# Kernel tuning notes

Hardware: AMD Instinct MI355X
Metric: run time of the kernel (lower is better)

The kernel has to match this reference:

```python
import jax, jax.numpy as jnp
import numpy as np
import math

VOCAB = 32000
D_MODEL = 1024
CTX = 2048
B, T = 4, 2048
NUM_Q_HEADS = 16
NUM_KV_GROUPS = 4
HEAD_DIM = D_MODEL // NUM_Q_HEADS          # 64
REP = NUM_Q_HEADS // NUM_KV_GROUPS         # queries per KV group = 4
HALF = D_MODEL // 2                        # token/pos embedding width


def setup_inputs() -> dict:
    key = jax.random.key(0)
    ks = jax.random.split(key, 12)
    s = 0.02
    idx = jax.random.randint(ks[0], (B, T), 0, VOCAB, dtype=jnp.int32)
    mask = jnp.tril(jnp.ones((T, T), dtype=jnp.int32))  # causal mask, 0 = blocked
    return {
        "idx": idx,
        "mask": mask,
        "tok_table": jax.random.normal(ks[1], (VOCAB, HALF), jnp.float32) * s,
        "pos_table": jax.random.normal(ks[2], (CTX, HALF), jnp.float32) * s,
        "W_q": jax.random.normal(ks[3], (D_MODEL, D_MODEL), jnp.float32) * s,
        "b_q": jnp.zeros((D_MODEL,), jnp.float32),
        "W_k": jax.random.normal(ks[4], (D_MODEL, NUM_KV_GROUPS * HEAD_DIM), jnp.float32) * s,
        "b_k": jnp.zeros((NUM_KV_GROUPS * HEAD_DIM,), jnp.float32),
        "W_v": jax.random.normal(ks[5], (D_MODEL, NUM_KV_GROUPS * HEAD_DIM), jnp.float32) * s,
        "b_v": jnp.zeros((NUM_KV_GROUPS * HEAD_DIM,), jnp.float32),
        "W_o": jax.random.normal(ks[6], (D_MODEL, D_MODEL), jnp.float32) * s,
        "b_o": jnp.zeros((D_MODEL,), jnp.float32),
    }


def reference(idx, mask, tok_table, pos_table, W_q, b_q, W_k, b_k, W_v, b_v, W_o, b_o):
    Bd, Td = idx.shape
    # token + position embedding, concatenated along feature dim -> [B, T, D_MODEL]
    tok_emb = tok_table[idx]                              # [B, T, HALF]
    pos_emb = pos_table[jnp.arange(Td)]                   # [T, HALF]
    x = jnp.concatenate([tok_emb, jnp.broadcast_to(pos_emb, (Bd, Td, HALF))], axis=-1)

    # GQA projections
    Q = (x @ W_q + b_q).reshape(Bd, Td, NUM_Q_HEADS, HEAD_DIM).transpose(0, 2, 1, 3)   # [B,H,T,D]
    K = (x @ W_k + b_k).reshape(Bd, Td, NUM_KV_GROUPS, HEAD_DIM).transpose(0, 2, 1, 3) # [B,G,T,D]
    V = (x @ W_v + b_v).reshape(Bd, Td, NUM_KV_GROUPS, HEAD_DIM).transpose(0, 2, 1, 3)
    # repeat_interleave KV groups to match query heads (naive GQA expansion)
    K = jnp.repeat(K, REP, axis=1)                        # [B,H,T,D]
    V = jnp.repeat(V, REP, axis=1)

    scale = 1.0 / math.sqrt(HEAD_DIM)
    scores = jnp.einsum('bhqd,bhkd->bhqk', Q, K) * scale  # [B,H,T,T]
    scores = jnp.where(mask == 0, jnp.float32(-1e9), scores)
    probs = jax.nn.softmax(scores, axis=-1)
    attn = jnp.einsum('bhqk,bhkd->bhqd', probs, V)        # [B,H,T,D]
    attn = attn.transpose(0, 2, 1, 3).reshape(Bd, Td, D_MODEL)
    return attn @ W_o + b_o
```

## Files before the change

kernel.cpp:

```cpp
#include <hip/hip_runtime.h>

typedef unsigned short u16;
typedef __attribute__((ext_vector_type(8))) short bf16x8;
typedef __attribute__((ext_vector_type(4))) float f32x4;

__device__ __forceinline__ u16 f2bf(float f) {
  union { float f; unsigned u; } x; x.f = f;
  unsigned r = x.u + 0x7fffu + ((x.u >> 16) & 1u);
  return (u16)(r >> 16);
}
__device__ __forceinline__ float bf2f(u16 u) {
  union { unsigned u; float f; } x; x.u = ((unsigned)u) << 16;
  return x.f;
}

#define GLOAD_LDS16(gp, lp)                                              \
  __builtin_amdgcn_global_load_lds(                                      \
      (const __attribute__((address_space(1))) unsigned int*)(gp),       \
      (__attribute__((address_space(3))) unsigned int*)(lp), 16, 0, 0)

__global__ __launch_bounds__(256) void transpose_w(const float* __restrict__ in,
                                                   u16* __restrict__ out, int N) {
  __shared__ float tile[32][33];
  const int n0 = blockIdx.x * 32, k0 = blockIdx.y * 32;
  const int tx = threadIdx.x & 31, ty = threadIdx.x >> 5;
#pragma unroll
  for (int i = 0; i < 4; ++i) {
    int k = k0 + ty + i * 8;
    tile[ty + i * 8][tx] = in[(size_t)k * N + n0 + tx];
  }
  __syncthreads();
#pragma unroll
  for (int i = 0; i < 4; ++i) {
    int n = n0 + ty + i * 8;
    out[(size_t)n * 1024 + k0 + tx] = f2bf(tile[tx][ty + i * 8]);
  }
}

__global__ __launch_bounds__(256) void embed_kernel(const int* __restrict__ idx,
                                                    const float* __restrict__ tok,
                                                    const float* __restrict__ pos,
                                                    u16* __restrict__ x) {
  const int r = blockIdx.x;
  const int t = r & 2047;
  const int tok_id = idx[r];
  const int c = threadIdx.x * 4;
  float4 v;
  if (c < 512)
    v = *(const float4*)&tok[(size_t)tok_id * 512 + c];
  else
    v = *(const float4*)&pos[(size_t)t * 512 + (c - 512)];
  ushort4 o;
  o.x = f2bf(v.x); o.y = f2bf(v.y); o.z = f2bf(v.z); o.w = f2bf(v.w);
  *(ushort4*)&x[(size_t)r * 1024 + c] = o;
}

__global__ __launch_bounds__(256) void gemm_qkv(const u16* __restrict__ A,
                                                const u16* __restrict__ Bt,
                                                const float* __restrict__ bq,
                                                const float* __restrict__ bk,
                                                const float* __restrict__ bv,
                                                u16* __restrict__ Qb, u16* __restrict__ Kb,
                                                u16* __restrict__ Vb) {
  __shared__ u16 Alds[128 * 32];
  __shared__ u16 Blds[128 * 32];
  const int tid = threadIdx.x;
  const int lane = tid & 63, w = tid >> 6;
  const int ln = lane & 15, lm = lane >> 4;
  const int wm = w & 1, wn = w >> 1;
  const int bm = blockIdx.y, bn = blockIdx.x;
  f32x4 acc[4][4] = {};
  const size_t arow0 = (size_t)bm * 128;
  const size_t brow0 = (size_t)bn * 128;
  for (int ks = 0; ks < 1024; ks += 32) {
    __syncthreads();
#pragma unroll
    for (int it = 0; it < 2; ++it) {
      const int idx = it * 256 + tid;
      const int row = idx >> 2, ko = idx & 3;
      GLOAD_LDS16(A + (arow0 + row) * 1024 + ks + ko * 8, &Alds[idx * 8]);
      GLOAD_LDS16(Bt + (brow0 + row) * 1024 + ks + ko * 8, &Blds[idx * 8]);
    }
    asm volatile("s_waitcnt vmcnt(0)" ::: "memory");
    __syncthreads();
    bf16x8 af[4], bfr[4];
#pragma unroll
    for (int m = 0; m < 4; ++m)
      af[m] = *(const bf16x8*)&Alds[(wm * 64 + m * 16 + ln) * 32 + lm * 8];
#pragma unroll
    for (int n = 0; n < 4; ++n)
      bfr[n] = *(const bf16x8*)&Blds[(wn * 64 + n * 16 + ln) * 32 + lm * 8];
#pragma unroll
    for (int m = 0; m < 4; ++m)
#pragma unroll
      for (int n = 0; n < 4; ++n)
        acc[m][n] = __builtin_amdgcn_mfma_f32_16x16x32_bf16(af[m], bfr[n], acc[m][n], 0, 0, 0);
  }
#pragma unroll
  for (int m = 0; m < 4; ++m) {
    const int rg0 = bm * 128 + wm * 64 + m * 16 + lm * 4;
#pragma unroll
    for (int n = 0; n < 4; ++n) {
      const int cg = bn * 128 + wn * 64 + n * 16 + ln;
      float bias;
      if (cg < 1024) bias = bq[cg];
      else if (cg < 1280) bias = bk[cg - 1024];
      else bias = bv[cg - 1280];
#pragma unroll
      for (int r = 0; r < 4; ++r) {
        const int rr = rg0 + r;
        const int bb = rr >> 11, tt = rr & 2047;
        const float v = acc[m][n][r] + bias;
        if (cg < 1024) {
          Qb[(((size_t)bb * 16 + (cg >> 6)) * 2048 + tt) * 64 + (cg & 63)] = f2bf(v);
        } else if (cg < 1280) {
          const int c2 = cg - 1024;
          Kb[(((size_t)bb * 4 + (c2 >> 6)) * 2048 + tt) * 64 + (c2 & 63)] = f2bf(v);
        } else {
          const int c2 = cg - 1280;
          Vb[(((size_t)bb * 4 + (c2 >> 6)) * 2048 + tt) * 64 + (c2 & 63)] = f2bf(v);
        }
      }
    }
  }
}

__global__ __launch_bounds__(256) void transpose_v(const u16* __restrict__ V,
                                                   u16* __restrict__ Vt) {
  __shared__ u16 tile[32][33];
  const int bg = blockIdx.z;
  const int d0 = blockIdx.x * 32, t0 = blockIdx.y * 32;
  const int tx = threadIdx.x & 31, ty = threadIdx.x >> 5;
  const u16* Vin = V + (size_t)bg * 2048 * 64;
  u16* Vout = Vt + (size_t)bg * 64 * 2048;
#pragma unroll
  for (int i = 0; i < 4; ++i)
    tile[ty + i * 8][tx] = Vin[(size_t)(t0 + ty + i * 8) * 64 + d0 + tx];
  __syncthreads();
#pragma unroll
  for (int i = 0; i < 4; ++i)
    Vout[(size_t)(d0 + ty + i * 8) * 2048 + t0 + tx] = tile[tx][ty + i * 8];
}

__global__ __launch_bounds__(256) void attn_kernel(const u16* __restrict__ Qb,
                                                   const u16* __restrict__ Kb,
                                                   const u16* __restrict__ Vt,
                                                   u16* __restrict__ attn) {
  __shared__ u16 Klds[32 * 64];
  __shared__ u16 Plds[4][16 * 32];
  const int tid = threadIdx.x;
  const int lane = tid & 63, w = tid >> 6;
  const int ln = lane & 15, lm = lane >> 4;
  const int qb = blockIdx.x;
  const int bh = blockIdx.y;
  const int b = bh >> 4, h = bh & 15, g = h >> 2;
  const u16* Qp = Qb + (size_t)bh * 2048 * 64;
  const u16* Kp = Kb + (size_t)(b * 4 + g) * 2048 * 64;
  const u16* Vp = Vt + (size_t)(b * 4 + g) * 64 * 2048;
  const int qw0 = qb * 64 + w * 16;

  bf16x8 qf[2];
  {
    const int qrow = qw0 + ln;
#pragma unroll
    for (int c = 0; c < 2; ++c) {
      bf16x8 raw = *(const bf16x8*)(Qp + (size_t)qrow * 64 + lm * 8 + c * 32);
#pragma unroll
      for (int i = 0; i < 8; ++i) raw[i] = (short)f2bf(bf2f((u16)raw[i]) * 0.125f);
      qf[c] = raw;
    }
  }

  f32x4 o[4] = {};
  float m_r[4], l_r[4];
#pragma unroll
  for (int r = 0; r < 4; ++r) { m_r[r] = -3.0e38f; l_r[r] = 0.0f; }

  const int nkb = (qb + 1) * 2;
  for (int kb = 0; kb < nkb; ++kb) {
    const int kv0 = kb * 32;
    __syncthreads();
    {
      const int row = tid >> 3, slot = tid & 7;
      const int sslot = slot ^ (row & 7);
      GLOAD_LDS16(Kp + (size_t)(kv0 + row) * 64 + sslot * 8, &Klds[tid * 8]);
    }
    asm volatile("s_waitcnt vmcnt(0)" ::: "memory");
    __syncthreads();

    if (kv0 <= qw0 + 15) {
      f32x4 s[2] = {};
#pragma unroll
      for (int n = 0; n < 2; ++n) {
        const int kr = n * 16 + ln;
#pragma unroll
        for (int c = 0; c < 2; ++c) {
          const int slot = lm + c * 4;
          bf16x8 kf = *(const bf16x8*)&Klds[kr * 64 + ((slot ^ (kr & 7)) * 8)];
          s[n] = __builtin_amdgcn_mfma_f32_16x16x32_bf16(qf[c], kf, s[n], 0, 0, 0);
        }
      }
#pragma unroll
      for (int n = 0; n < 2; ++n)
#pragma unroll
        for (int r = 0; r < 4; ++r) {
          const int kv = kv0 + n * 16 + ln;
          const int q = qw0 + lm * 4 + r;
          if (kv > q) s[n][r] = -1.0e30f;
        }
      float mx[4];
#pragma unroll
      for (int r = 0; r < 4; ++r) mx[r] = fmaxf(s[0][r], s[1][r]);
#pragma unroll
      for (int off = 1; off < 16; off <<= 1)
#pragma unroll
        for (int r = 0; r < 4; ++r) mx[r] = fmaxf(mx[r], __shfl_xor(mx[r], off));
      float corr[4];
#pragma unroll
      for (int r = 0; r < 4; ++r) {
        const float mnew = fmaxf(m_r[r], mx[r]);
        corr[r] = __expf(m_r[r] - mnew);
        m_r[r] = mnew;
      }
#pragma unroll
      for (int n = 0; n < 2; ++n)
#pragma unroll
        for (int r = 0; r < 4; ++r) s[n][r] = __expf(s[n][r] - m_r[r]);
      float sum[4];
#pragma unroll
      for (int r = 0; r < 4; ++r) sum[r] = s[0][r] + s[1][r];
#pragma unroll
      for (int off = 1; off < 16; off <<= 1)
#pragma unroll
        for (int r = 0; r < 4; ++r) sum[r] += __shfl_xor(sum[r], off);
#pragma unroll
      for (int r = 0; r < 4; ++r) l_r[r] = l_r[r] * corr[r] + sum[r];
#pragma unroll
      for (int nd = 0; nd < 4; ++nd)
#pragma unroll
        for (int r = 0; r < 4; ++r) o[nd][r] *= corr[r];
#pragma unroll
      for (int n = 0; n < 2; ++n)
#pragma unroll
        for (int r = 0; r < 4; ++r)
          Plds[w][(lm * 4 + r) * 32 + n * 16 + ln] = f2bf(s[n][r]);
      asm volatile("s_waitcnt lgkmcnt(0)" ::: "memory");
      const bf16x8 pf = *(const bf16x8*)&Plds[w][ln * 32 + lm * 8];
#pragma unroll
      for (int nd = 0; nd < 4; ++nd) {
        const bf16x8 vf = *(const bf16x8*)(Vp + (size_t)(nd * 16 + ln) * 2048 + kv0 + lm * 8);
        o[nd] = __builtin_amdgcn_mfma_f32_16x16x32_bf16(pf, vf, o[nd], 0, 0, 0);
      }
    }
  }
  float invl[4];
#pragma unroll
  for (int r = 0; r < 4; ++r) invl[r] = 1.0f / l_r[r];
#pragma unroll
  for (int nd = 0; nd < 4; ++nd)
#pragma unroll
    for (int r = 0; r < 4; ++r) {
      const int q = qw0 + lm * 4 + r;
      const int col = h * 64 + nd * 16 + ln;
      attn[((size_t)b * 2048 + q) * 1024 + col] = f2bf(o[nd][r] * invl[r]);
    }
}

__global__ __launch_bounds__(256) void gemm_out(const u16* __restrict__ A,
                                                const u16* __restrict__ Bt,
                                                const float* __restrict__ bo,
                                                float* __restrict__ out) {
  __shared__ u16 Alds[128 * 32];
  __shared__ u16 Blds[128 * 32];
  const int tid = threadIdx.x;
  const int lane = tid & 63, w = tid >> 6;
  const int ln = lane & 15, lm = lane >> 4;
  const int wm = w & 1, wn = w >> 1;
  const int bm = blockIdx.y, bn = blockIdx.x;
  f32x4 acc[4][4] = {};
  const size_t arow0 = (size_t)bm * 128;
  const size_t brow0 = (size_t)bn * 128;
  for (int ks = 0; ks < 1024; ks += 32) {
    __syncthreads();
#pragma unroll
    for (int it = 0; it < 2; ++it) {
      const int idx = it * 256 + tid;
      const int row = idx >> 2, ko = idx & 3;
      GLOAD_LDS16(A + (arow0 + row) * 1024 + ks + ko * 8, &Alds[idx * 8]);
      GLOAD_LDS16(Bt + (brow0 + row) * 1024 + ks + ko * 8, &Blds[idx * 8]);
    }
    asm volatile("s_waitcnt vmcnt(0)" ::: "memory");
    __syncthreads();
    bf16x8 af[4], bfr[4];
#pragma unroll
    for (int m = 0; m < 4; ++m)
      af[m] = *(const bf16x8*)&Alds[(wm * 64 + m * 16 + ln) * 32 + lm * 8];
#pragma unroll
    for (int n = 0; n < 4; ++n)
      bfr[n] = *(const bf16x8*)&Blds[(wn * 64 + n * 16 + ln) * 32 + lm * 8];
#pragma unroll
    for (int m = 0; m < 4; ++m)
#pragma unroll
      for (int n = 0; n < 4; ++n)
        acc[m][n] = __builtin_amdgcn_mfma_f32_16x16x32_bf16(af[m], bfr[n], acc[m][n], 0, 0, 0);
  }
#pragma unroll
  for (int m = 0; m < 4; ++m) {
    const int rg0 = bm * 128 + wm * 64 + m * 16 + lm * 4;
#pragma unroll
    for (int n = 0; n < 4; ++n) {
      const int cg = bn * 128 + wn * 64 + n * 16 + ln;
      const float bias = bo[cg];
#pragma unroll
      for (int r = 0; r < 4; ++r)
        out[(size_t)(rg0 + r) * 1024 + cg] = acc[m][n][r] + bias;
    }
  }
}

extern "C" void kernel_launch(void* const* d_in, const int* in_sizes, int n_in,
                              void* d_out, int out_size, void* d_ws, size_t ws_size,
                              hipStream_t stream) {
  const int* idx = (const int*)d_in[0];
  const float* tok = (const float*)d_in[2];
  const float* pos = (const float*)d_in[3];
  const float* Wq = (const float*)d_in[4];
  const float* bq = (const float*)d_in[5];
  const float* Wk = (const float*)d_in[6];
  const float* bk = (const float*)d_in[7];
  const float* Wv = (const float*)d_in[8];
  const float* bv = (const float*)d_in[9];
  const float* Wo = (const float*)d_in[10];
  const float* bo = (const float*)d_in[11];
  float* out = (float*)d_out;

  char* ws = (char*)d_ws;
  u16* x_bf   = (u16*)(ws);
  u16* wqkv_t = (u16*)(ws + 16777216);
  u16* wo_t   = (u16*)(ws + 19922944);
  u16* Qb     = (u16*)(ws + 22020096);
  u16* Kb     = (u16*)(ws + 38797312);
  u16* Vb     = (u16*)(ws + 42991616);
  u16* Vt     = (u16*)(ws + 47185920);

  transpose_w<<<dim3(32, 32), 256, 0, stream>>>(Wq, wqkv_t, 1024);
  transpose_w<<<dim3(8, 32), 256, 0, stream>>>(Wk, wqkv_t + (size_t)1024 * 1024, 256);
  transpose_w<<<dim3(8, 32), 256, 0, stream>>>(Wv, wqkv_t + (size_t)1280 * 1024, 256);
  transpose_w<<<dim3(32, 32), 256, 0, stream>>>(Wo, wo_t, 1024);
  embed_kernel<<<8192, 256, 0, stream>>>(idx, tok, pos, x_bf);
  gemm_qkv<<<dim3(12, 64), 256, 0, stream>>>(x_bf, wqkv_t, bq, bk, bv, Qb, Kb, Vb);
  transpose_v<<<dim3(2, 64, 16), 256, 0, stream>>>(Vb, Vt);
  attn_kernel<<<dim3(32, 64), 256, 0, stream>>>(Qb, Kb, Vt, x_bf);
  gemm_out<<<dim3(8, 64), 256, 0, stream>>>(x_bf, wo_t, bo, out);
}
```

Measured before the change: 522.3 us.

## Pair causal query tiles per block and read K directly from global

Each attention block now handles two query tiles, pair and 31-pair, so every block does about the same amount of causal work and the grid is halved. The shared K tile, its barriers and the vmcnt waits are removed. Each wave now reads K fragments straight from global memory and loops only over its own causal extent, so waves no longer wait on each other. The P scratch in LDS gets an XOR swizzle to cut bank conflicts. The cost is that K is no longer shared through LDS across the four waves, which raises global and L2 traffic, and the grid has fewer blocks.

Measured after the change: 452.5 us. 1.15x faster.

```diff
diff --git a/kernel.cpp b/kernel.cpp
--- a/kernel.cpp
+++ b/kernel.cpp
@@ -146,57 +146,49 @@
                                                    const u16* __restrict__ Kb,
                                                    const u16* __restrict__ Vt,
                                                    u16* __restrict__ attn) {
-  __shared__ u16 Klds[32 * 64];
   __shared__ u16 Plds[4][16 * 32];
   const int tid = threadIdx.x;
   const int lane = tid & 63, w = tid >> 6;
   const int ln = lane & 15, lm = lane >> 4;
-  const int qb = blockIdx.x;
+  const int pair = blockIdx.x;
   const int bh = blockIdx.y;
   const int b = bh >> 4, h = bh & 15, g = h >> 2;
   const u16* Qp = Qb + (size_t)bh * 2048 * 64;
   const u16* Kp = Kb + (size_t)(b * 4 + g) * 2048 * 64;
   const u16* Vp = Vt + (size_t)(b * 4 + g) * 64 * 2048;
-  const int qw0 = qb * 64 + w * 16;
-
-  bf16x8 qf[2];
-  {
-    const int qrow = qw0 + ln;
-#pragma unroll
-    for (int c = 0; c < 2; ++c) {
-      bf16x8 raw = *(const bf16x8*)(Qp + (size_t)qrow * 64 + lm * 8 + c * 32);
-#pragma unroll
-      for (int i = 0; i < 8; ++i) raw[i] = (short)f2bf(bf2f((u16)raw[i]) * 0.125f);
-      qf[c] = raw;
-    }
-  }
-
-  f32x4 o[4] = {};
-  float m_r[4], l_r[4];
-#pragma unroll
-  for (int r = 0; r < 4; ++r) { m_r[r] = -3.0e38f; l_r[r] = 0.0f; }
-
-  const int nkb = (qb + 1) * 2;
-  for (int kb = 0; kb < nkb; ++kb) {
-    const int kv0 = kb * 32;
-    __syncthreads();
+
+#pragma unroll
+  for (int half = 0; half < 2; ++half) {
+    const int qt = half ? (31 - pair) : pair;
+    const int qw0 = qt * 64 + w * 16;
+
+    bf16x8 qf[2];
     {
-      const int row = tid >> 3, slot = tid & 7;
-      const int sslot = slot ^ (row & 7);
-      GLOAD_LDS16(Kp + (size_t)(kv0 + row) * 64 + sslot * 8, &Klds[tid * 8]);
-    }
-    asm volatile("s_waitcnt vmcnt(0)" ::: "memory");
-    __syncthreads();
-
-    if (kv0 <= qw0 + 15) {
+      const int qrow = qw0 + ln;
+#pragma unroll
+      for (int c = 0; c < 2; ++c) {
+        bf16x8 raw = *(const bf16x8*)(Qp + (size_t)qrow * 64 + c * 32 + lm * 8);
+#pragma unroll
+        for (int i = 0; i < 8; ++i) raw[i] = (short)f2bf(bf2f((u16)raw[i]) * 0.125f);
+        qf[c] = raw;
+      }
+    }
+
+    f32x4 o[4] = {};
+    float m_r[4], l_r[4];
+#pragma unroll
+    for (int r = 0; r < 4; ++r) { m_r[r] = -3.0e38f; l_r[r] = 0.0f; }
+
+    const int my_nkb = (qw0 >> 5) + 1;
+    for (int kb = 0; kb < my_nkb; ++kb) {
+      const int kv0 = kb * 32;
       f32x4 s[2] = {};
 #pragma unroll
       for (int n = 0; n < 2; ++n) {
-        const int kr = n * 16 + ln;
 #pragma unroll
         for (int c = 0; c < 2; ++c) {
-          const int slot = lm + c * 4;
-          bf16x8 kf = *(const bf16x8*)&Klds[kr * 64 + ((slot ^ (kr & 7)) * 8)];
+          const bf16x8 kf =
+              *(const bf16x8*)(Kp + (size_t)(kv0 + n * 16 + ln) * 64 + c * 32 + lm * 8);
           s[n] = __builtin_amdgcn_mfma_f32_16x16x32_bf16(qf[c], kf, s[n], 0, 0, 0);
         }
       }
@@ -242,28 +234,32 @@
 #pragma unroll
       for (int n = 0; n < 2; ++n)
 #pragma unroll
-        for (int r = 0; r < 4; ++r)
-          Plds[w][(lm * 4 + r) * 32 + n * 16 + ln] = f2bf(s[n][r]);
+        for (int r = 0; r < 4; ++r) {
+          const int row = lm * 4 + r, col = n * 16 + ln;
+          const int slot = (col >> 3) ^ ((row >> 1) & 3);
+          Plds[w][row * 32 + slot * 8 + (col & 7)] = f2bf(s[n][r]);
+        }
       asm volatile("s_waitcnt lgkmcnt(0)" ::: "memory");
-      const bf16x8 pf = *(const bf16x8*)&Plds[w][ln * 32 + lm * 8];
+      const bf16x8 pf = *(const bf16x8*)&Plds[w][ln * 32 + (lm ^ ((ln >> 1) & 3)) * 8];
 #pragma unroll
       for (int nd = 0; nd < 4; ++nd) {
-        const bf16x8 vf = *(const bf16x8*)(Vp + (size_t)(nd * 16 + ln) * 2048 + kv0 + lm * 8);
+        const bf16x8 vf =
+            *(const bf16x8*)(Vp + (size_t)(nd * 16 + ln) * 2048 + kv0 + lm * 8);
         o[nd] = __builtin_amdgcn_mfma_f32_16x16x32_bf16(pf, vf, o[nd], 0, 0, 0);
       }
     }
-  }
-  float invl[4];
-#pragma unroll
-  for (int r = 0; r < 4; ++r) invl[r] = 1.0f / l_r[r];
-#pragma unroll
-  for (int nd = 0; nd < 4; ++nd)
-#pragma unroll
-    for (int r = 0; r < 4; ++r) {
-      const int q = qw0 + lm * 4 + r;
-      const int col = h * 64 + nd * 16 + ln;
-      attn[((size_t)b * 2048 + q) * 1024 + col] = f2bf(o[nd][r] * invl[r]);
-    }
+    float invl[4];
+#pragma unroll
+    for (int r = 0; r < 4; ++r) invl[r] = 1.0f / l_r[r];
+#pragma unroll
+    for (int nd = 0; nd < 4; ++nd)
+#pragma unroll
+      for (int r = 0; r < 4; ++r) {
+        const int q = qw0 + lm * 4 + r;
+        const int col = h * 64 + nd * 16 + ln;
+        attn[((size_t)b * 2048 + q) * 1024 + col] = f2bf(o[nd][r] * invl[r]);
+      }
+  }
 }
 
 __global__ __launch_bounds__(256) void gemm_out(const u16* __restrict__ A,
@@ -350,6 +346,6 @@
   embed_kernel<<<8192, 256, 0, stream>>>(idx, tok, pos, x_bf);
   gemm_qkv<<<dim3(12, 64), 256, 0, stream>>>(x_bf, wqkv_t, bq, bk, bv, Qb, Kb, Vb);
   transpose_v<<<dim3(2, 64, 16), 256, 0, stream>>>(Vb, Vt);
-  attn_kernel<<<dim3(32, 64), 256, 0, stream>>>(Qb, Kb, Vt, x_bf);
+  attn_kernel<<<dim3(16, 64), 256, 0, stream>>>(Qb, Kb, Vt, x_bf);
   gemm_out<<<dim3(8, 64), 256, 0, stream>>>(x_bf, wo_t, bo, out);
 }
```
